# Performance work log

Hardware: AMD Instinct MI355X
Metric: run time of the kernel (lower is better)

## Reference

```python
import jax, jax.numpy as jnp
import numpy as np

DIM = 1024
NUM_HEADS = 16
HEAD_DIM = DIM // NUM_HEADS
ROPE_BASE = 10000.0


def _rope_cos_sin(seq_len, head_dim, dtype):
    inv_freq = 1.0 / (ROPE_BASE ** (jnp.arange(0, head_dim, 2, dtype=jnp.float32) / head_dim))
    t = jnp.arange(seq_len, dtype=jnp.float32)
    freqs = jnp.einsum('i,j->ij', t, inv_freq)          # (S, head_dim/2)
    emb = jnp.concatenate([freqs, freqs], axis=-1)       # (S, head_dim)
    return jnp.cos(emb).astype(dtype), jnp.sin(emb).astype(dtype)


def _rotate_half(x):
    x1, x2 = jnp.split(x, 2, axis=-1)
    return jnp.concatenate([-x2, x1], axis=-1)


def setup_inputs() -> dict:
    key = jax.random.key(0)
    k1, k2, k3 = jax.random.split(key, 3)
    B, S = 2, 2048
    x = jax.random.normal(k1, (B, S, DIM), dtype=jnp.float32)
    w_qkv = jax.random.normal(k2, (3 * DIM, DIM), dtype=jnp.float32) * (DIM ** -0.5)
    w_out = jax.random.normal(k3, (DIM, DIM), dtype=jnp.float32) * (DIM ** -0.5)
    return {"x": x, "w_qkv": w_qkv, "w_out": w_out}


def reference(x, w_qkv, w_out):
    B, S, _ = x.shape
    scale = HEAD_DIM ** -0.5

    qkv = jnp.einsum('bsd,ed->bse', x, w_qkv)                 # (B, S, 3*DIM)
    qkv = qkv.reshape(B, S, 3, NUM_HEADS, HEAD_DIM)
    qkv = jnp.transpose(qkv, (2, 0, 3, 1, 4))                  # (3, B, H, S, hd)
    Q, K, V = qkv[0], qkv[1], qkv[2]

    cos, sin = _rope_cos_sin(S, HEAD_DIM, x.dtype)             # (S, hd)
    Q = Q * cos + _rotate_half(Q) * sin
    K = K * cos + _rotate_half(K) * sin

    scores = jnp.einsum('bhqd,bhkd->bhqk', Q, K) * scale       # (B, H, S, S)
    causal = jnp.tril(jnp.ones((S, S), dtype=bool))
    scores = jnp.where(causal[None, None], scores, jnp.asarray(-1e9, scores.dtype))
    attn = jax.nn.softmax(scores, axis=-1)

    out = jnp.einsum('bhqk,bhkd->bhqd', attn, V)               # (B, H, S, hd)
    out = jnp.transpose(out, (0, 2, 1, 3)).reshape(B, S, DIM)
    out = jnp.einsum('bsd,ed->bse', out, w_out)
    return out
```

## Files before the change

### kernel.cpp

```cpp
#include <hip/hip_runtime.h>
#include <hip/hip_bf16.h>

#define DIM 1024
#define NHEADS 16
#define HD 64
#define BB 2
#define SS 2048
#define MTOT (BB*SS)
#define SCALE 0.125f
#define QSCALE 0.1803368801111204f

typedef __attribute__((ext_vector_type(8))) short bf16x8;
typedef __attribute__((ext_vector_type(4))) float f32x4;

__device__ __forceinline__ float bf2f(short u) {
  union { float f; unsigned int i; } v;
  v.i = ((unsigned int)(unsigned short)u) << 16;
  return v.f;
}
__device__ __forceinline__ short f2bf(float f) {
  union { float f; unsigned int i; } v; v.f = f;
  unsigned int r = v.i + 0x7fffu + ((v.i >> 16) & 1u);
  return (short)(r >> 16);
}
__device__ __forceinline__ unsigned int cvtpk_bf16(float lo, float hi) {
  unsigned int r;
  asm("v_cvt_pk_bf16_f32 %0, %1, %2" : "=v"(r) : "v"(lo), "v"(hi));
  return r;
}
__device__ __forceinline__ void async_load16(const short* g, short* l) {
  __builtin_amdgcn_global_load_lds(
      (const __attribute__((address_space(1))) unsigned int*)g,
      (__attribute__((address_space(3))) unsigned int*)l, 16, 0, 0);
}

__global__ void cvt3_kernel(const float* __restrict__ a, short* __restrict__ oa, int na,
                            const float* __restrict__ b, short* __restrict__ ob, int nb,
                            const float* __restrict__ c, short* __restrict__ oc, int nc,
                            float* __restrict__ ct, float* __restrict__ st) {
  int gid = blockIdx.x * blockDim.x + threadIdx.x;
  if (gid < SS * 32) {
    int s = gid >> 5, j = gid & 31;
    float inv = 1.0f / powf(10000.0f, (float)(2 * j) / 64.0f);
    float ang = (float)s * inv;
    ct[gid] = cosf(ang);
    st[gid] = sinf(ang);
  }
  int stride = gridDim.x * blockDim.x;
  int tot = na + nb + nc;
  for (int q = gid; q < tot; q += stride) {
    const float* src; short* dst; int off;
    if (q < na)            { src = a; dst = oa; off = q; }
    else if (q < na + nb)  { src = b; dst = ob; off = q - na; }
    else                   { src = c; dst = oc; off = q - na - nb; }
    float4 v = *(const float4*)(src + (size_t)off * 4);
    short4 o;
    o.x = f2bf(v.x); o.y = f2bf(v.y); o.z = f2bf(v.z); o.w = f2bf(v.w);
    *(short4*)(dst + (size_t)off * 4) = o;
  }
}

template<int BN, bool OUT_F32>
__global__ __launch_bounds__(256) void gemm_bt(
    const short* __restrict__ A, const short* __restrict__ B,
    void* __restrict__ C, int M, int N, int K) {
  constexpr int NFR = BN / 32;
  __shared__ __align__(16) short As[128][32];
  __shared__ __align__(16) short Bs[BN][32];
  const int nbx = N / BN;
  const int chunk = gridDim.x >> 3;
  const int wg = (blockIdx.x & 7) * chunk + (blockIdx.x >> 3);
  const int m0 = (wg / nbx) * 128, n0 = (wg % nbx) * BN;
  const int tid = threadIdx.x;
  const int lane = tid & 63;
  const int wid = tid >> 6;
  const int wm = (wid >> 1) * 64, wn = (wid & 1) * (BN / 2);
  const int row = lane & 15, kg = (lane >> 4) * 8;
  const int lrow = lane >> 2;
  const int lcol = (lane & 3) * 8;

  f32x4 acc[4][NFR];
#pragma unroll
  for (int m = 0; m < 4; m++)
#pragma unroll
    for (int n = 0; n < NFR; n++) acc[m][n] = (f32x4){0.f, 0.f, 0.f, 0.f};

  for (int kk = 0; kk < K; kk += 32) {
    __syncthreads();
#pragma unroll
    for (int i = 0; i < 2; i++) {
      int base = i * 64 + wid * 16;
      async_load16(A + (size_t)(m0 + base + lrow) * K + kk + lcol, &As[base][0]);
    }
    if constexpr (BN == 128) {
#pragma unroll
      for (int i = 0; i < 2; i++) {
        int base = i * 64 + wid * 16;
        async_load16(B + (size_t)(n0 + base + lrow) * K + kk + lcol, &Bs[base][0]);
      }
    } else {
      int base = wid * 16;
      async_load16(B + (size_t)(n0 + base + lrow) * K + kk + lcol, &Bs[base][0]);
    }
    __syncthreads();
    bf16x8 af[4], bfr[NFR];
#pragma unroll
    for (int m = 0; m < 4; m++) af[m] = *(const bf16x8*)(&As[wm + m * 16 + row][kg]);
#pragma unroll
    for (int n = 0; n < NFR; n++) bfr[n] = *(const bf16x8*)(&Bs[wn + n * 16 + row][kg]);
#pragma unroll
    for (int m = 0; m < 4; m++)
#pragma unroll
      for (int n = 0; n < NFR; n++)
        acc[m][n] = __builtin_amdgcn_mfma_f32_16x16x32_bf16(af[m], bfr[n], acc[m][n], 0, 0, 0);
  }
  const int orow = (lane >> 4) * 4, ocol = lane & 15;
#pragma unroll
  for (int m = 0; m < 4; m++)
#pragma unroll
    for (int n = 0; n < NFR; n++)
#pragma unroll
      for (int r = 0; r < 4; r++) {
        int gr = m0 + wm + m * 16 + orow + r;
        int gc = n0 + wn + n * 16 + ocol;
        if (OUT_F32) ((float*)C)[(size_t)gr * N + gc] = acc[m][n][r];
        else         ((short*)C)[(size_t)gr * N + gc] = f2bf(acc[m][n][r]);
      }
}

__global__ __launch_bounds__(256) void ropev_kernel(
    const short* __restrict__ qkv, const float* __restrict__ ct, const float* __restrict__ st,
    short* __restrict__ Q, short* __restrict__ K, short* __restrict__ Vt) {
  int bh = blockIdx.y;
  int b = bh >> 4, h = bh & 15;
  int t = threadIdx.x;
  if (blockIdx.x < SS / 64) {
    int s0 = blockIdx.x * 64;
    int rl = t >> 2;
    int d8 = (t & 3) * 8;
    int s = s0 + rl;
    size_t inbase = ((size_t)(b * SS + s)) * 3072 + h * 64 + d8;
    size_t outbase = ((size_t)bh * SS + s) * 64;
    float c[8], sn[8];
#pragma unroll
    for (int j = 0; j < 8; j++) { c[j] = ct[s * 32 + d8 + j]; sn[j] = st[s * 32 + d8 + j]; }
    {
      bf16x8 x1 = *(const bf16x8*)(qkv + inbase);
      bf16x8 x2 = *(const bf16x8*)(qkv + inbase + 32);
      bf16x8 o1, o2;
#pragma unroll
      for (int j = 0; j < 8; j++) {
        float a = bf2f(x1[j]), bb = bf2f(x2[j]);
        o1[j] = f2bf((a * c[j] - bb * sn[j]) * QSCALE);
        o2[j] = f2bf((bb * c[j] + a * sn[j]) * QSCALE);
      }
      *(bf16x8*)(Q + outbase + d8) = o1;
      *(bf16x8*)(Q + outbase + d8 + 32) = o2;
    }
    {
      bf16x8 x1 = *(const bf16x8*)(qkv + inbase + 1024);
      bf16x8 x2 = *(const bf16x8*)(qkv + inbase + 1024 + 32);
      bf16x8 o1, o2;
#pragma unroll
      for (int j = 0; j < 8; j++) {
        float a = bf2f(x1[j]), bb = bf2f(x2[j]);
        o1[j] = f2bf(a * c[j] - bb * sn[j]);
        o2[j] = f2bf(bb * c[j] + a * sn[j]);
      }
      int pc = (t & 3) ^ (s & 7);
      *(bf16x8*)(K + outbase + pc * 8) = o1;
      *(bf16x8*)(K + outbase + (pc ^ 4) * 8) = o2;
    }
  } else {
    __shared__ short ls[64][72];
    int s0 = (blockIdx.x - SS / 64) * 64;
#pragma unroll
    for (int p = 0; p < 2; p++) {
      int idx = p * 256 + t;
      int r = idx >> 3, c8 = (idx & 7) * 8;
      *(bf16x8*)(&ls[r][c8]) =
          *(const bf16x8*)(qkv + ((size_t)(b * SS + s0 + r)) * 3072 + 2048 + h * 64 + c8);
    }
    __syncthreads();
    int dl = t >> 2, sg = (t & 3) * 16;
    int c = sg >> 5, hi = (sg >> 4) & 1;
    short tmp[16];
#pragma unroll
    for (int j = 0; j < 16; j++) tmp[j] = ls[sg + j][dl];
    size_t rowbase = ((size_t)bh * 64 + dl) * SS + s0;
#pragma unroll
    for (int g = 0; g < 4; g++) {
      short4 o = { tmp[4 * g], tmp[4 * g + 1], tmp[4 * g + 2], tmp[4 * g + 3] };
      int pc = (c * 4 + g) ^ (dl & 7);
      *(short4*)(Vt + rowbase + pc * 8 + hi * 4) = o;
    }
  }
}

__global__ __launch_bounds__(256, 6) void attn_kernel(
    const short* __restrict__ Qp, const short* __restrict__ Kp, const short* __restrict__ Vt,
    short* __restrict__ O, float* __restrict__ Pf) {
  __shared__ __align__(16) short KsF[2][64 * 64];
  __shared__ __align__(16) short VsF[2][64 * 64];
  int flat = blockIdx.x;
  int wk = (flat & 7) * 128 + (flat >> 3);
  int bh = wk >> 5;
  int sub = wk & 31;
  int pr = sub >> 1, half = sub & 1;
  int b = bh >> 4, h = bh & 15;
  int tid = threadIdx.x, lane = tid & 63, w = tid >> 6;
  int row = lane & 15, grp = lane >> 4;
  const int qtH = 31 - pr;
  const int nseg = 1 + half;
  const int ck = (grp ^ (row & 7)) * 8;

  const short* Kbase = Kp + (size_t)bh * SS * 64;
  const short* Vbase = Vt + (size_t)bh * 64 * SS;
  const int sr8 = lane >> 3;
  const int sc8 = (lane & 7) * 8;

  auto STAGE = [&](int bufi, int kv0) {
#pragma unroll
    for (int i = 0; i < 2; i++) {
      int rbase = i * 32 + w * 8;
      async_load16(Kbase + (size_t)(kv0 + rbase + sr8) * 64 + sc8, &KsF[bufi][rbase * 64]);
      async_load16(Vbase + (size_t)(rbase + sr8) * SS + kv0 + sc8, &VsF[bufi][rbase * 64]);
    }
  };

  const int kts0 = half ? 16 : 0;
  int cur = 0;
  STAGE(0, kts0 * 64);

#pragma unroll 1
  for (int s = 0; s < nseg; s++) {
    const int qt  = (s == 0) ? qtH : pr;
    const int kts = (s == 0) ? kts0 : 0;
    const int kte = (s == 0) ? (half ? qtH : 15) : pr;
    const bool fin = (s == 1);
    const int q0 = qt * 64;
    const int q = q0 + w * 16 + row;
    bf16x8 qf0, qf1;
    {
      size_t qb = ((size_t)bh * SS + q) * 64 + grp * 8;
      qf0 = *(const bf16x8*)(Qp + qb);
      qf1 = *(const bf16x8*)(Qp + qb + 32);
    }
    f32x4 acc[4];
#pragma unroll
    for (int d = 0; d < 4; d++) acc[d] = (f32x4){0.f, 0.f, 0.f, 0.f};
    float m = -1e30f, l = 0.f;

#pragma unroll 1
    for (int kt = kts; kt <= kte; kt++) {
      int kv0 = kt * 64;
      bool more = (kt < kte) || (s + 1 < nseg);
      if (more) {
        STAGE(cur ^ 1, kt < kte ? kv0 + 64 : 0);
        asm volatile("s_waitcnt vmcnt(4)" ::: "memory");
      } else {
        asm volatile("s_waitcnt vmcnt(0)" ::: "memory");
      }
      __builtin_amdgcn_sched_barrier(0);
      __builtin_amdgcn_s_barrier();
      __builtin_amdgcn_sched_barrier(0);
      const short* Kc = &KsF[cur][0];
      const short* Vc = &VsF[cur][0];

      bool last = (kt == qt);
      float sv[4][4];
      __builtin_amdgcn_s_setprio(1);
#pragma unroll
      for (int n = 0; n < 4; n++) {
        if (last && n > w) {
#pragma unroll
          for (int r = 0; r < 4; r++) sv[n][r] = -1e30f;
          continue;
        }
        f32x4 sf = (f32x4){0.f, 0.f, 0.f, 0.f};
        const short* kr_ = Kc + (n * 16 + row) * 64;
        bf16x8 kf0 = *(const bf16x8*)(kr_ + ck);
        bf16x8 kf1 = *(const bf16x8*)(kr_ + (ck ^ 32));
        sf = __builtin_amdgcn_mfma_f32_16x16x32_bf16(kf0, qf0, sf, 0, 0, 0);
        sf = __builtin_amdgcn_mfma_f32_16x16x32_bf16(kf1, qf1, sf, 0, 0, 0);
#pragma unroll
        for (int r = 0; r < 4; r++) sv[n][r] = sf[r];
      }
      __builtin_amdgcn_s_setprio(0);
      if (last) {
#pragma unroll
        for (int n = 0; n < 4; n++)
#pragma unroll
          for (int r = 0; r < 4; r++) {
            int kv = kv0 + n * 16 + grp * 4 + r;
            if (kv > q) sv[n][r] = -1e30f;
          }
      }
      float pmax = -1e30f;
#pragma unroll
      for (int n = 0; n < 4; n++)
#pragma unroll
        for (int r = 0; r < 4; r++) pmax = fmaxf(pmax, sv[n][r]);
      pmax = fmaxf(pmax, __shfl_xor(pmax, 16));
      pmax = fmaxf(pmax, __shfl_xor(pmax, 32));
      if (__any(pmax - m > 8.f)) {
        float mnew = fmaxf(m, pmax);
        float resc = __builtin_amdgcn_exp2f(m - mnew);
        m = mnew;
        l *= resc;
#pragma unroll
        for (int d = 0; d < 4; d++)
#pragma unroll
          for (int r = 0; r < 4; r++) acc[d][r] *= resc;
      }
      float psum = 0.f;
#pragma unroll
      for (int n = 0; n < 4; n++)
#pragma unroll
        for (int r = 0; r < 4; r++) {
          float pv = __builtin_amdgcn_exp2f(sv[n][r] - m);
          sv[n][r] = pv;
          psum += pv;
        }
      psum += __shfl_xor(psum, 16);
      psum += __shfl_xor(psum, 32);
      l += psum;
      __builtin_amdgcn_s_setprio(1);
#pragma unroll
      for (int c = 0; c < 2; c++) {
        union { unsigned int u[4]; bf16x8 v; } pu;
        pu.u[0] = cvtpk_bf16(sv[2 * c][0], sv[2 * c][1]);
        pu.u[1] = cvtpk_bf16(sv[2 * c][2], sv[2 * c][3]);
        pu.u[2] = cvtpk_bf16(sv[2 * c + 1][0], sv[2 * c + 1][1]);
        pu.u[3] = cvtpk_bf16(sv[2 * c + 1][2], sv[2 * c + 1][3]);
#pragma unroll
        for (int dm = 0; dm < 4; dm++) {
          const short* vr_ = Vc + (dm * 16 + row) * 64;
          bf16x8 vf = *(const bf16x8*)(vr_ + (ck ^ (c * 32)));
          acc[dm] = __builtin_amdgcn_mfma_f32_16x16x32_bf16(vf, pu.v, acc[dm], 0, 0, 0);
        }
      }
      __builtin_amdgcn_s_setprio(0);
      __builtin_amdgcn_sched_barrier(0);
      __builtin_amdgcn_s_barrier();
      __builtin_amdgcn_sched_barrier(0);
      cur ^= 1;
    }
    if (fin) {
      float linv = 1.0f / l;
      size_t ob = ((size_t)(b * SS + q)) * 1024 + h * 64 + grp * 4;
#pragma unroll
      for (int dm = 0; dm < 4; dm++) {
        union { unsigned int u[2]; short4 s4; } ou;
        ou.u[0] = cvtpk_bf16(acc[dm][0] * linv, acc[dm][1] * linv);
        ou.u[1] = cvtpk_bf16(acc[dm][2] * linv, acc[dm][3] * linv);
        *(short4*)(O + ob + dm * 16) = ou.s4;
      }
    } else {
      int slot = (bh * 16 + (qt - 16)) * 2 + half;
      float* P = Pf + (size_t)slot * 64 * 68 + (w * 16 + row) * 68;
#pragma unroll
      for (int dm = 0; dm < 4; dm++) {
        f32x4 a = acc[dm];
        *(float4*)(P + dm * 16 + grp * 4) = *(float4*)&a;
      }
      if (grp == 0) { P[64] = m; P[65] = l; }
    }
  }
}

__global__ __launch_bounds__(64) void merge_kernel(const float* __restrict__ Pf, short* __restrict__ O) {
  int bh = blockIdx.x >> 4, ht = blockIdx.x & 15;
  int b = bh >> 4, h = bh & 15;
  int qt = ht + 16;
  int t = threadIdx.x;
  const float* p0 = Pf + ((size_t)((bh * 16 + ht) * 2)) * 64 * 68 + t * 68;
  const float* p1 = p0 + 64 * 68;
  float m0 = p0[64], l0 = p0[65], m1 = p1[64], l1 = p1[65];
  float mM = fmaxf(m0, m1);
  float e0 = __builtin_amdgcn_exp2f(m0 - mM);
  float e1 = __builtin_amdgcn_exp2f(m1 - mM);
  float linv = 1.0f / (e0 * l0 + e1 * l1);
  size_t ob = ((size_t)(b * SS + qt * 64 + t)) * 1024 + h * 64;
#pragma unroll
  for (int d8 = 0; d8 < 8; d8++) {
    float4 a0 = *(const float4*)(p0 + d8 * 8);
    float4 a1 = *(const float4*)(p1 + d8 * 8);
    float4 b0 = *(const float4*)(p0 + d8 * 8 + 4);
    float4 b1 = *(const float4*)(p1 + d8 * 8 + 4);
    union { unsigned int u[4]; short4 s4[2]; } ou;
    ou.u[0] = cvtpk_bf16((e0 * a0.x + e1 * a1.x) * linv, (e0 * a0.y + e1 * a1.y) * linv);
    ou.u[1] = cvtpk_bf16((e0 * a0.z + e1 * a1.z) * linv, (e0 * a0.w + e1 * a1.w) * linv);
    ou.u[2] = cvtpk_bf16((e0 * b0.x + e1 * b1.x) * linv, (e0 * b0.y + e1 * b1.y) * linv);
    ou.u[3] = cvtpk_bf16((e0 * b0.z + e1 * b1.z) * linv, (e0 * b0.w + e1 * b1.w) * linv);
    *(short4*)(O + ob + d8 * 8) = ou.s4[0];
    *(short4*)(O + ob + d8 * 8 + 4) = ou.s4[1];
  }
}

extern "C" void kernel_launch(void* const* d_in, const int* in_sizes, int n_in,
                              void* d_out, int out_size, void* d_ws, size_t ws_size,
                              hipStream_t stream) {
  (void)in_sizes; (void)n_in; (void)out_size; (void)ws_size;
  const float* x     = (const float*)d_in[0];
  const float* w_qkv = (const float*)d_in[1];
  const float* w_out = (const float*)d_in[2];
  float* out = (float*)d_out;

  char* ws = (char*)d_ws;
  size_t off = 0;
  auto alloc = [&](size_t bytes) -> void* {
    void* p = ws + off;
    off += (bytes + 255) & ~(size_t)255;
    return p;
  };
  short* xb    = (short*)alloc((size_t)MTOT * DIM * 2);
  short* wqkvb = (short*)alloc((size_t)3072 * 1024 * 2);
  short* woutb = (short*)alloc((size_t)1024 * 1024 * 2);
  short* qkvb  = (short*)alloc((size_t)MTOT * 3072 * 2);
  short* Qb    = (short*)alloc((size_t)32 * SS * 64 * 2);
  short* Kb    = (short*)alloc((size_t)32 * SS * 64 * 2);
  short* Vtb   = (short*)alloc((size_t)32 * 64 * SS * 2);
  float* ct    = (float*)alloc((size_t)SS * 32 * 4);
  float* st    = (float*)alloc((size_t)SS * 32 * 4);
  short* attnb = xb;
  float* Pf    = (float*)qkvb;

  cvt3_kernel<<<2048, 256, 0, stream>>>(x, xb, MTOT * DIM / 4,
                                        w_qkv, wqkvb, 3072 * 1024 / 4,
                                        w_out, woutb, 1024 * 1024 / 4, ct, st);
  gemm_bt<128, false><<<(3072 / 128) * (MTOT / 128), 256, 0, stream>>>(xb, wqkvb, qkvb, MTOT, 3072, 1024);
  ropev_kernel<<<dim3(2 * SS / 64, 32), 256, 0, stream>>>(qkvb, ct, st, Qb, Kb, Vtb);
  attn_kernel<<<1024, 256, 0, stream>>>(Qb, Kb, Vtb, attnb, Pf);
  merge_kernel<<<512, 64, 0, stream>>>(Pf, attnb);
  gemm_bt<64, true><<<(1024 / 64) * (MTOT / 128), 256, 0, stream>>>(attnb, woutb, out, MTOT, 1024, 1024);
}
```

Baseline: 128.8 us.

## Fuse RoPE and V transpose into QKV GEMM epilogue; compute row sums via MFMA

```diff
diff --git a/kernel.cpp b/kernel.cpp
--- a/kernel.cpp
+++ b/kernel.cpp
@@ -57,6 +57,101 @@
     short4 o;
     o.x = f2bf(v.x); o.y = f2bf(v.y); o.z = f2bf(v.z); o.w = f2bf(v.w);
     *(short4*)(dst + (size_t)off * 4) = o;
+  }
+}
+
+__global__ __launch_bounds__(256) void gemm_qkv(
+    const short* __restrict__ A, const short* __restrict__ B,
+    const float* __restrict__ ct, const float* __restrict__ st,
+    short* __restrict__ Q, short* __restrict__ K, short* __restrict__ Vt) {
+  constexpr int N = 3072, Kd = 1024;
+  __shared__ __align__(16) short As[128][32];
+  __shared__ __align__(16) short Bs[128][32];
+  const int nbx = N >> 7;
+  const int chunk = gridDim.x >> 3;
+  const int wg = (blockIdx.x & 7) * chunk + (blockIdx.x >> 3);
+  const int m0 = (wg / nbx) * 128, n0 = (wg % nbx) * 128;
+  const int tid = threadIdx.x;
+  const int lane = tid & 63;
+  const int wid = tid >> 6;
+  const int wm = (wid >> 1) * 64, wn = (wid & 1) * 64;
+  const int row = lane & 15, kg = (lane >> 4) * 8;
+  const int lrow = lane >> 2;
+  const int lcol = (lane & 3) * 8;
+
+  f32x4 acc[4][4];
+#pragma unroll
+  for (int m = 0; m < 4; m++)
+#pragma unroll
+    for (int n = 0; n < 4; n++) acc[m][n] = (f32x4){0.f, 0.f, 0.f, 0.f};
+
+  for (int kk = 0; kk < Kd; kk += 32) {
+    __syncthreads();
+#pragma unroll
+    for (int i = 0; i < 2; i++) {
+      int base = i * 64 + wid * 16;
+      async_load16(A + (size_t)(m0 + base + lrow) * Kd + kk + lcol, &As[base][0]);
+      async_load16(B + (size_t)(n0 + base + lrow) * Kd + kk + lcol, &Bs[base][0]);
+    }
+    __syncthreads();
+    bf16x8 af[4], bfr[4];
+#pragma unroll
+    for (int m = 0; m < 4; m++) af[m] = *(const bf16x8*)(&As[wm + m * 16 + row][kg]);
+#pragma unroll
+    for (int n = 0; n < 4; n++) bfr[n] = *(const bf16x8*)(&Bs[wn + n * 16 + row][kg]);
+#pragma unroll
+    for (int m = 0; m < 4; m++)
+#pragma unroll
+      for (int n = 0; n < 4; n++)
+        acc[m][n] = __builtin_amdgcn_mfma_f32_16x16x32_bf16(af[m], bfr[n], acc[m][n], 0, 0, 0);
+  }
+  const int orow = (lane >> 4) * 4, ocol = lane & 15;
+  const int region = n0 >> 10;
+  const int e0 = n0 & 1023;
+  if (region < 2) {
+#pragma unroll
+    for (int m = 0; m < 4; m++) {
+      int gr0 = m0 + wm + m * 16 + orow;
+#pragma unroll
+      for (int n = 0; n < 2; n++) {
+        int e = e0 + wn + n * 16 + ocol;
+        int h = e >> 6, dd = e & 63;
+#pragma unroll
+        for (int r = 0; r < 4; r++) {
+          int g = gr0 + r, s = g & (SS - 1), b = g >> 11;
+          float cv = ct[s * 32 + dd], sv_ = st[s * 32 + dd];
+          float a = acc[m][n][r], bb = acc[m][n + 2][r];
+          float o1 = a * cv - bb * sv_;
+          float o2 = bb * cv + a * sv_;
+          size_t base = ((size_t)((b * 16 + h) * SS + s)) * 64;
+          if (region == 0) {
+            Q[base + dd]      = f2bf(o1 * QSCALE);
+            Q[base + dd + 32] = f2bf(o2 * QSCALE);
+          } else {
+            int pc = (dd >> 3) ^ (s & 7);
+            K[base + pc * 8 + (dd & 7)]       = f2bf(o1);
+            K[base + (pc ^ 4) * 8 + (dd & 7)] = f2bf(o2);
+          }
+        }
+      }
+    }
+  } else {
+#pragma unroll
+    for (int m = 0; m < 4; m++) {
+      int gr0 = m0 + wm + m * 16 + orow;
+      int s0 = gr0 & (SS - 1), b = gr0 >> 11;
+      int c = (s0 >> 5) & 1, hi = (s0 >> 4) & 1, gg = (s0 >> 2) & 3;
+#pragma unroll
+      for (int n = 0; n < 4; n++) {
+        int e = e0 + wn + n * 16 + ocol;
+        int h = e >> 6, dd = e & 63;
+        int pchunk = (c * 4 + gg) ^ (dd & 7);
+        union { unsigned int u[2]; short4 s4; } ou;
+        ou.u[0] = cvtpk_bf16(acc[m][n][0], acc[m][n][1]);
+        ou.u[1] = cvtpk_bf16(acc[m][n][2], acc[m][n][3]);
+        *(short4*)(Vt + ((size_t)((b * 16 + h) * 64 + dd)) * SS + (s0 & ~63) + pchunk * 8 + hi * 4) = ou.s4;
+      }
+    }
   }
 }
 
@@ -128,75 +223,6 @@
       }
 }
 
-__global__ __launch_bounds__(256) void ropev_kernel(
-    const short* __restrict__ qkv, const float* __restrict__ ct, const float* __restrict__ st,
-    short* __restrict__ Q, short* __restrict__ K, short* __restrict__ Vt) {
-  int bh = blockIdx.y;
-  int b = bh >> 4, h = bh & 15;
-  int t = threadIdx.x;
-  if (blockIdx.x < SS / 64) {
-    int s0 = blockIdx.x * 64;
-    int rl = t >> 2;
-    int d8 = (t & 3) * 8;
-    int s = s0 + rl;
-    size_t inbase = ((size_t)(b * SS + s)) * 3072 + h * 64 + d8;
-    size_t outbase = ((size_t)bh * SS + s) * 64;
-    float c[8], sn[8];
-#pragma unroll
-    for (int j = 0; j < 8; j++) { c[j] = ct[s * 32 + d8 + j]; sn[j] = st[s * 32 + d8 + j]; }
-    {
-      bf16x8 x1 = *(const bf16x8*)(qkv + inbase);
-      bf16x8 x2 = *(const bf16x8*)(qkv + inbase + 32);
-      bf16x8 o1, o2;
-#pragma unroll
-      for (int j = 0; j < 8; j++) {
-        float a = bf2f(x1[j]), bb = bf2f(x2[j]);
-        o1[j] = f2bf((a * c[j] - bb * sn[j]) * QSCALE);
-        o2[j] = f2bf((bb * c[j] + a * sn[j]) * QSCALE);
-      }
-      *(bf16x8*)(Q + outbase + d8) = o1;
-      *(bf16x8*)(Q + outbase + d8 + 32) = o2;
-    }
-    {
-      bf16x8 x1 = *(const bf16x8*)(qkv + inbase + 1024);
-      bf16x8 x2 = *(const bf16x8*)(qkv + inbase + 1024 + 32);
-      bf16x8 o1, o2;
-#pragma unroll
-      for (int j = 0; j < 8; j++) {
-        float a = bf2f(x1[j]), bb = bf2f(x2[j]);
-        o1[j] = f2bf(a * c[j] - bb * sn[j]);
-        o2[j] = f2bf(bb * c[j] + a * sn[j]);
-      }
-      int pc = (t & 3) ^ (s & 7);
-      *(bf16x8*)(K + outbase + pc * 8) = o1;
-      *(bf16x8*)(K + outbase + (pc ^ 4) * 8) = o2;
-    }
-  } else {
-    __shared__ short ls[64][72];
-    int s0 = (blockIdx.x - SS / 64) * 64;
-#pragma unroll
-    for (int p = 0; p < 2; p++) {
-      int idx = p * 256 + t;
-      int r = idx >> 3, c8 = (idx & 7) * 8;
-      *(bf16x8*)(&ls[r][c8]) =
-          *(const bf16x8*)(qkv + ((size_t)(b * SS + s0 + r)) * 3072 + 2048 + h * 64 + c8);
-    }
-    __syncthreads();
-    int dl = t >> 2, sg = (t & 3) * 16;
-    int c = sg >> 5, hi = (sg >> 4) & 1;
-    short tmp[16];
-#pragma unroll
-    for (int j = 0; j < 16; j++) tmp[j] = ls[sg + j][dl];
-    size_t rowbase = ((size_t)bh * 64 + dl) * SS + s0;
-#pragma unroll
-    for (int g = 0; g < 4; g++) {
-      short4 o = { tmp[4 * g], tmp[4 * g + 1], tmp[4 * g + 2], tmp[4 * g + 3] };
-      int pc = (c * 4 + g) ^ (dl & 7);
-      *(short4*)(Vt + rowbase + pc * 8 + hi * 4) = o;
-    }
-  }
-}
-
 __global__ __launch_bounds__(256, 6) void attn_kernel(
     const short* __restrict__ Qp, const short* __restrict__ Kp, const short* __restrict__ Vt,
     short* __restrict__ O, float* __restrict__ Pf) {
@@ -213,6 +239,8 @@
   const int qtH = 31 - pr;
   const int nseg = 1 + half;
   const int ck = (grp ^ (row & 7)) * 8;
+  const short one_bf = (short)0x3F80;
+  const bf16x8 ones = {one_bf, one_bf, one_bf, one_bf, one_bf, one_bf, one_bf, one_bf};
 
   const short* Kbase = Kp + (size_t)bh * SS * 64;
   const short* Vbase = Vt + (size_t)bh * 64 * SS;
@@ -247,9 +275,10 @@
       qf1 = *(const bf16x8*)(Qp + qb + 32);
     }
     f32x4 acc[4];
+    f32x4 acc2 = (f32x4){0.f, 0.f, 0.f, 0.f};
 #pragma unroll
     for (int d = 0; d < 4; d++) acc[d] = (f32x4){0.f, 0.f, 0.f, 0.f};
-    float m = -1e30f, l = 0.f;
+    float m = -1e30f;
 
 #pragma unroll 1
     for (int kt = kts; kt <= kte; kt++) {
@@ -296,35 +325,30 @@
             if (kv > q) sv[n][r] = -1e30f;
           }
       }
-      float pmax = -1e30f;
-#pragma unroll
-      for (int n = 0; n < 4; n++)
-#pragma unroll
-        for (int r = 0; r < 4; r++) pmax = fmaxf(pmax, sv[n][r]);
+      float t0 = fmaxf(fmaxf(sv[0][0], sv[0][1]), sv[0][2]);
+      float t1 = fmaxf(fmaxf(sv[0][3], sv[1][0]), sv[1][1]);
+      float t2 = fmaxf(fmaxf(sv[1][2], sv[1][3]), sv[2][0]);
+      float t3 = fmaxf(fmaxf(sv[2][1], sv[2][2]), sv[2][3]);
+      float t4 = fmaxf(fmaxf(sv[3][0], sv[3][1]), sv[3][2]);
+      float pmax = fmaxf(fmaxf(fmaxf(t0, t1), fmaxf(t2, t3)), fmaxf(t4, sv[3][3]));
       pmax = fmaxf(pmax, __shfl_xor(pmax, 16));
       pmax = fmaxf(pmax, __shfl_xor(pmax, 32));
       if (__any(pmax - m > 8.f)) {
         float mnew = fmaxf(m, pmax);
         float resc = __builtin_amdgcn_exp2f(m - mnew);
         m = mnew;
-        l *= resc;
 #pragma unroll
         for (int d = 0; d < 4; d++)
 #pragma unroll
           for (int r = 0; r < 4; r++) acc[d][r] *= resc;
-      }
-      float psum = 0.f;
+#pragma unroll
+        for (int r = 0; r < 4; r++) acc2[r] *= resc;
+      }
 #pragma unroll
       for (int n = 0; n < 4; n++)
 #pragma unroll
-        for (int r = 0; r < 4; r++) {
-          float pv = __builtin_amdgcn_exp2f(sv[n][r] - m);
-          sv[n][r] = pv;
-          psum += pv;
-        }
-      psum += __shfl_xor(psum, 16);
-      psum += __shfl_xor(psum, 32);
-      l += psum;
+        for (int r = 0; r < 4; r++)
+          sv[n][r] = __builtin_amdgcn_exp2f(sv[n][r] - m);
       __builtin_amdgcn_s_setprio(1);
 #pragma unroll
       for (int c = 0; c < 2; c++) {
@@ -339,6 +363,7 @@
           bf16x8 vf = *(const bf16x8*)(vr_ + (ck ^ (c * 32)));
           acc[dm] = __builtin_amdgcn_mfma_f32_16x16x32_bf16(vf, pu.v, acc[dm], 0, 0, 0);
         }
+        acc2 = __builtin_amdgcn_mfma_f32_16x16x32_bf16(ones, pu.v, acc2, 0, 0, 0);
       }
       __builtin_amdgcn_s_setprio(0);
       __builtin_amdgcn_sched_barrier(0);
@@ -347,7 +372,7 @@
       cur ^= 1;
     }
     if (fin) {
-      float linv = 1.0f / l;
+      float linv = 1.0f / acc2[0];
       size_t ob = ((size_t)(b * SS + q)) * 1024 + h * 64 + grp * 4;
 #pragma unroll
       for (int dm = 0; dm < 4; dm++) {
@@ -364,7 +389,7 @@
         f32x4 a = acc[dm];
         *(float4*)(P + dm * 16 + grp * 4) = *(float4*)&a;
       }
-      if (grp == 0) { P[64] = m; P[65] = l; }
+      if (grp == 0) { P[64] = m; P[65] = acc2[0]; }
     }
   }
 }
@@ -417,20 +442,18 @@
   short* xb    = (short*)alloc((size_t)MTOT * DIM * 2);
   short* wqkvb = (short*)alloc((size_t)3072 * 1024 * 2);
   short* woutb = (short*)alloc((size_t)1024 * 1024 * 2);
-  short* qkvb  = (short*)alloc((size_t)MTOT * 3072 * 2);
+  float* Pf    = (float*)alloc((size_t)32 * 16 * 2 * 64 * 68 * 4);
   short* Qb    = (short*)alloc((size_t)32 * SS * 64 * 2);
   short* Kb    = (short*)alloc((size_t)32 * SS * 64 * 2);
   short* Vtb   = (short*)alloc((size_t)32 * 64 * SS * 2);
   float* ct    = (float*)alloc((size_t)SS * 32 * 4);
   float* st    = (float*)alloc((size_t)SS * 32 * 4);
   short* attnb = xb;
-  float* Pf    = (float*)qkvb;
 
   cvt3_kernel<<<2048, 256, 0, stream>>>(x, xb, MTOT * DIM / 4,
                                         w_qkv, wqkvb, 3072 * 1024 / 4,
                                         w_out, woutb, 1024 * 1024 / 4, ct, st);
-  gemm_bt<128, false><<<(3072 / 128) * (MTOT / 128), 256, 0, stream>>>(xb, wqkvb, qkvb, MTOT, 3072, 1024);
-  ropev_kernel<<<dim3(2 * SS / 64, 32), 256, 0, stream>>>(qkvb, ct, st, Qb, Kb, Vtb);
+  gemm_qkv<<<(3072 / 128) * (MTOT / 128), 256, 0, stream>>>(xb, wqkvb, ct, st, Qb, Kb, Vtb);
   attn_kernel<<<1024, 256, 0, stream>>>(Qb, Kb, Vtb, attnb, Pf);
   merge_kernel<<<512, 64, 0, stream>>>(Pf, attnb);
   gemm_bt<64, true><<<(1024 / 64) * (MTOT / 128), 256, 0, stream>>>(attnb, woutb, out, MTOT, 1024, 1024);
```

Result: slower. 140.6 us (+9.1%).
